# Kernel optimization log

Hardware: AMD Instinct MI355X
Metric: run time of the kernel (lower is better)

Reference implementation:

```python
import jax, jax.numpy as jnp
import numpy as np

TAU_RANK = 0.5
GAMMA_RANK = 1.0
TAU_GATE = 1.0
LN_EPS = 1e-5


def setup_inputs() -> dict:
    key = jax.random.key(0)
    ks = jax.random.split(key, 8)
    B, L, D, H, V = 8, 2048, 768, 1024, 32000
    ids = jax.random.randint(ks[0], (B, L), 0, V)
    embeddings = jax.random.normal(ks[1], (B, L, D), dtype=jnp.float32)
    attn = (jax.random.uniform(ks[2], (B, L)) < 0.9).astype(jnp.float32)
    rhos = jnp.array([0.1, 0.25, 0.5], dtype=jnp.float32)
    ln_g = jnp.ones((D,), jnp.float32)
    ln_b = jnp.zeros((D,), jnp.float32)
    w1 = jax.random.normal(ks[3], (D, H), dtype=jnp.float32) * 0.02
    b1 = jnp.zeros((H,), jnp.float32)
    w2 = jax.random.normal(ks[4], (H, 1), dtype=jnp.float32) * 0.02
    b2 = jnp.zeros((1,), jnp.float32)
    emb_table = jax.random.normal(ks[5], (V, D), dtype=jnp.float32) * 0.02
    return {"ids": ids, "embeddings": embeddings, "attn": attn, "rhos": rhos,
            "ln_g": ln_g, "ln_b": ln_b, "w1": w1, "b1": b1, "w2": w2, "b2": b2,
            "emb_table": emb_table}


def _selector_mlp(x, ln_g, ln_b, w1, b1, w2, b2):
    mu = x.mean(-1, keepdims=True)
    var = ((x - mu) ** 2).mean(-1, keepdims=True)
    x = (x - mu) / jnp.sqrt(var + LN_EPS) * ln_g + ln_b
    x = jax.nn.gelu(x @ w1 + b1, approximate=False)  # dropout eval = identity
    return (x @ w2 + b2)[..., 0]  # [B, L]


def _pool(emb, attn):
    # masked mean pooling: [.., L, D], [.., L] -> [.., D]
    denom = jnp.maximum(attn.sum(-1, keepdims=True), 1.0)
    return (emb * attn[..., None]).sum(-2) / denom


def _soft_rank(scores, attn, tau, gamma=1.0):
    scores = jnp.where(attn == 0, 0.0, scores)
    denom = jnp.maximum(attn.sum(1, keepdims=True), 1.0)
    mean = (scores * attn).sum(1, keepdims=True) / denom
    var = (((scores - mean) ** 2) * attn).sum(1, keepdims=True) / denom
    s = (scores - mean) / jnp.sqrt(var + 1e-6)
    # diff[b,i,j] = s[b,i] - s[b,j]
    p = jax.nn.sigmoid(-(s[:, :, None] - s[:, None, :]) / tau)
    if gamma != 1.0:
        p = p ** gamma
    p = p * (attn[:, None, :] * attn[:, :, None])
    r = 0.5 + p.sum(2)
    return jnp.where(attn == 0, 1e9, r)


def reference(ids, embeddings, attn, rhos, ln_g, ln_b, w1, b1, w2, b2, emb_table):
    attn_f = attn.astype(jnp.float32)
    emb = embeddings * attn_f[..., None]
    scores = _selector_mlp(emb, ln_g, ln_b, w1, b1, w2, b2)
    scores = jnp.where(attn_f == 0, 0.0, scores)

    full_rep = jax.lax.stop_gradient(_pool(embeddings, attn_f))  # [B, D]
    L_eff = attn_f.sum(1)  # [B]
    ranks = _soft_rank(scores, attn_f, TAU_RANK, GAMMA_RANK)  # [B, L]

    B, L = ids.shape
    R = rhos.shape[0]
    k = jnp.round(rhos[:, None] * L_eff[None]).astype(jnp.int32)  # [R, B]
    k = jnp.where(L_eff[None] > 0, jnp.maximum(k, 1), 0)
    k_f = k.astype(jnp.float32)

    gate_raw = jax.nn.sigmoid((k_f[:, :, None] - ranks[None]) / TAU_GATE) * attn_f[None]
    z = gate_raw / jnp.maximum(gate_raw.sum(-1, keepdims=True), 1e-8)
    z = z * k_f[:, :, None]  # [R, B, L]

    invalid_ranks = jnp.where(attn_f == 0, jnp.inf, ranks)
    # rank position of each token = inverse of the sort permutation
    rank_pos = jnp.argsort(jnp.argsort(invalid_ranks, axis=1), axis=1)  # [B, L]
    g = (rank_pos[None] < k[:, :, None]).astype(jnp.float32)  # hard top-k gate [R, B, L]

    g_st = g + (z - jax.lax.stop_gradient(z))  # straight-through
    effective_attn = attn_f[None] * g_st  # [R, B, L]

    tok = emb_table[ids]  # [B, L, D]; shared across R
    pred_rep = _pool(tok[None], effective_attn)  # [R, B, D]

    eps = 1e-8
    num = (pred_rep * full_rep[None]).sum(-1)
    den = jnp.maximum(jnp.linalg.norm(pred_rep, axis=-1), eps) * \
          jnp.maximum(jnp.linalg.norm(full_rep[None] * jnp.ones_like(pred_rep[..., :1]), axis=-1), eps)
    cos = num / den
    loss = (1.0 - cos).mean()
    return z, g, loss
```

## Files before the change

kernel.cpp:

```cpp
#include <hip/hip_runtime.h>
#include <math.h>

#define NB 8
#define NL 2048
#define ND 768
#define NH 1024
#define NR 3
#define NM (NB*NL)
#define LS 32
#define LOG2E  1.4426950408889634f
#define LOG2E2 2.8853900817779268f

typedef _Float16 h16;
typedef __attribute__((ext_vector_type(2))) _Float16 h16x2;
typedef __attribute__((ext_vector_type(8))) _Float16 h16x8;
typedef __attribute__((ext_vector_type(4))) float f32x4;

#define ASCALE 4.0f
#define BSCALE 64.0f
#define INV_AB (1.0f/(ASCALE*BSCALE))

enum : int {
  WS_SCORES = 0,
  WS_MU     = WS_SCORES + NM,
  WS_ISTD   = WS_MU + NM,
  WS_LEFF   = WS_ISTD + NM,
  WS_SMEAN  = WS_LEFF + 8,
  WS_SISTD  = WS_SMEAN + 8,
  WS_KF     = WS_SISTD + 8,
  WS_GDEN   = WS_KF + 24,
  WS_LOSSP  = WS_GDEN + 24,
  WS_CBP    = WS_LOSSP + 24,
  WS_SPART  = WS_CBP + 24*NH,
  WS_FPART  = WS_SPART + 16*NM,
  WS_PPART  = WS_FPART + LS*NB*ND,
  WS_RPART  = WS_PPART + LS*NR*NB*ND,
  WS_POSP   = WS_RPART + 4*NM,
  WS_BTH    = WS_POSP + 4*NM,
  WS_BTL    = WS_BTH + NH*ND/2,
  WS_END    = WS_BTL + NH*ND/2
};

__device__ __forceinline__ float block_sum256(float v) {
  __shared__ float tmp[4];
  __shared__ float res;
  int lane = threadIdx.x & 63;
  int w = threadIdx.x >> 6;
  #pragma unroll
  for (int o = 32; o > 0; o >>= 1) v += __shfl_down(v, o);
  if (lane == 0) tmp[w] = v;
  __syncthreads();
  if (threadIdx.x == 0) res = tmp[0] + tmp[1] + tmp[2] + tmp[3];
  __syncthreads();
  return res;
}

__device__ __forceinline__ void f16split2(float a, float b, h16x2& hi, h16x2& lo) {
  auto h = __builtin_amdgcn_cvt_pkrtz(a, b);
  float ra = a - (float)h[0];
  float rb = b - (float)h[1];
  auto l = __builtin_amdgcn_cvt_pkrtz(ra, rb);
  hi = (h16x2){(h16)h[0], (h16)h[1]};
  lo = (h16x2){(h16)l[0], (h16)l[1]};
}

__device__ __forceinline__ float fsig_exp2(float x) {
  return __builtin_amdgcn_rcpf(1.f + exp2f(x));
}

__global__ void k_stats(const float* __restrict__ emb, const float* __restrict__ attn,
                        float* __restrict__ ws) {
  int w = threadIdx.x >> 6, l = threadIdx.x & 63;
  int m = blockIdx.x*4 + w;
  const float* x = emb + (size_t)m * ND;
  float a = attn[m];
  float4 v0 = *(const float4*)&x[l*4];
  float4 v1 = *(const float4*)&x[256 + l*4];
  float4 v2 = *(const float4*)&x[512 + l*4];
  float s = v0.x+v0.y+v0.z+v0.w + v1.x+v1.y+v1.z+v1.w + v2.x+v2.y+v2.z+v2.w;
  #pragma unroll
  for (int o = 1; o < 64; o <<= 1) s += __shfl_xor(s, o);
  float mu = a * s / (float)ND;
  float q = 0.f;
  float xs[12] = {v0.x,v0.y,v0.z,v0.w, v1.x,v1.y,v1.z,v1.w, v2.x,v2.y,v2.z,v2.w};
  #pragma unroll
  for (int e = 0; e < 12; ++e) { float d = xs[e]*a - mu; q = fmaf(d, d, q); }
  #pragma unroll
  for (int o = 1; o < 64; o <<= 1) q += __shfl_xor(q, o);
  if (l == 0) {
    ws[WS_MU + m] = mu;
    ws[WS_ISTD + m] = 1.f / sqrtf(q / (float)ND + 1e-5f);
  }
}

__global__ void k_fullpart(const float* __restrict__ emb, const float* __restrict__ attn,
                           float* __restrict__ ws) {
  int b = blockIdx.x, dc = blockIdx.y, ls = blockIdx.z;
  int d = dc*256 + threadIdx.x;
  float acc = 0.f;
  int l0 = ls * (NL/LS);
  for (int l = l0; l < l0 + NL/LS; ++l)
    acc = fmaf(emb[((size_t)(b*NL + l))*ND + d], attn[b*NL + l], acc);
  ws[WS_FPART + ls*(NB*ND) + b*ND + d] = acc;
}

__global__ void k_splitBcb(const float* __restrict__ w1, const float* __restrict__ lng,
                           const float* __restrict__ lnb, float* __restrict__ ws) {
  __shared__ float tile[32][33];
  int bk = blockIdx.x, bn = blockIdx.y, t = threadIdx.x;
  int i = t >> 5, j = t & 31;
  #pragma unroll
  for (int s = 0; s < 4; ++s)
    tile[i + 8*s][j] = w1[(size_t)(bk*32 + i + 8*s)*NH + bn*32 + j];
  __syncthreads();
  h16* bth = (h16*)(ws + WS_BTH);
  h16* btl = (h16*)(ws + WS_BTL);
  int kl = j;
  float lg = lng[bk*32 + kl] * BSCALE;
  #pragma unroll
  for (int s = 0; s < 4; ++s) {
    int nl = i + 8*s;
    int n = bn*32 + nl, k = bk*32 + kl;
    float v = tile[kl][nl] * lg;
    h16 hi = (h16)v;
    bth[(size_t)n*ND + k] = hi;
    btl[(size_t)n*ND + k] = (h16)(v - (float)hi);
  }
  if (t < 32) {
    float s = 0.f;
    #pragma unroll
    for (int kl2 = 0; kl2 < 32; ++kl2)
      s = fmaf(lnb[bk*32 + kl2], tile[kl2][t], s);
    ws[WS_CBP + bk*NH + bn*32 + t] = s;
  }
}

__global__ void __launch_bounds__(256) k_gemm(
    const float* __restrict__ emb, const float* __restrict__ attn,
    const float* __restrict__ b1, const float* __restrict__ w2,
    float* __restrict__ ws) {
  __shared__ h16 AsH[128][36], AsL[128][36], BsH[128][36], BsL[128][36];
  int t = threadIdx.x;
  int m0 = blockIdx.x * 128, n0 = blockIdx.y * 128;
  int ar = t >> 1, ak = (t & 1) * 16;
  float isv = ws[WS_ISTD + m0 + ar];
  float pco  = ASCALE * attn[m0 + ar] * isv;
  float mqco = -ASCALE * ws[WS_MU + m0 + ar] * isv;
  int lane = t & 63, w = t >> 6, wm = w >> 1, wn = w & 1;
  int fr = lane & 15, g = lane >> 4;
  f32x4 acc[4][4];
  #pragma unroll
  for (int i = 0; i < 4; ++i)
    #pragma unroll
    for (int j = 0; j < 4; ++j) acc[i][j] = (f32x4){0.f, 0.f, 0.f, 0.f};
  const h16* bth = (const h16*)(ws + WS_BTH);
  const h16* btl = (const h16*)(ws + WS_BTL);

  for (int k0 = 0; k0 < ND; k0 += 32) {
    h16 hs[16], lo[16];
    #pragma unroll
    for (int i = 0; i < 2; ++i) {
      float4 x0 = *(const float4*)&emb[(size_t)(m0 + ar)*ND + k0 + ak + 8*i];
      float4 x1 = *(const float4*)&emb[(size_t)(m0 + ar)*ND + k0 + ak + 8*i + 4];
      h16x2 h0, l0v, h1, l1, h2, l2, h3, l3;
      f16split2(fmaf(x0.x, pco, mqco), fmaf(x0.y, pco, mqco), h0, l0v);
      f16split2(fmaf(x0.z, pco, mqco), fmaf(x0.w, pco, mqco), h1, l1);
      f16split2(fmaf(x1.x, pco, mqco), fmaf(x1.y, pco, mqco), h2, l2);
      f16split2(fmaf(x1.z, pco, mqco), fmaf(x1.w, pco, mqco), h3, l3);
      hs[8*i+0]=h0[0]; hs[8*i+1]=h0[1]; hs[8*i+2]=h1[0]; hs[8*i+3]=h1[1];
      hs[8*i+4]=h2[0]; hs[8*i+5]=h2[1]; hs[8*i+6]=h3[0]; hs[8*i+7]=h3[1];
      lo[8*i+0]=l0v[0]; lo[8*i+1]=l0v[1]; lo[8*i+2]=l1[0]; lo[8*i+3]=l1[1];
      lo[8*i+4]=l2[0]; lo[8*i+5]=l2[1]; lo[8*i+6]=l3[0]; lo[8*i+7]=l3[1];
    }
    h16x8 bh0 = *(const h16x8*)&bth[(size_t)(n0 + ar)*ND + k0 + ak];
    h16x8 bh1 = *(const h16x8*)&bth[(size_t)(n0 + ar)*ND + k0 + ak + 8];
    h16x8 bl0 = *(const h16x8*)&btl[(size_t)(n0 + ar)*ND + k0 + ak];
    h16x8 bl1 = *(const h16x8*)&btl[(size_t)(n0 + ar)*ND + k0 + ak + 8];
    __syncthreads();
    *(h16x8*)&AsH[ar][ak]     = *(const h16x8*)&hs[0];
    *(h16x8*)&AsH[ar][ak + 8] = *(const h16x8*)&hs[8];
    *(h16x8*)&AsL[ar][ak]     = *(const h16x8*)&lo[0];
    *(h16x8*)&AsL[ar][ak + 8] = *(const h16x8*)&lo[8];
    *(h16x8*)&BsH[ar][ak]     = bh0;
    *(h16x8*)&BsH[ar][ak + 8] = bh1;
    *(h16x8*)&BsL[ar][ak]     = bl0;
    *(h16x8*)&BsL[ar][ak + 8] = bl1;
    __syncthreads();
    h16x8 ah[4], al[4];
    #pragma unroll
    for (int mi = 0; mi < 4; ++mi) {
      int r = wm*64 + mi*16 + fr;
      ah[mi] = *(const h16x8*)&AsH[r][g*8];
      al[mi] = *(const h16x8*)&AsL[r][g*8];
    }
    #pragma unroll
    for (int ni = 0; ni < 4; ++ni) {
      int c = wn*64 + ni*16 + fr;
      h16x8 bh = *(const h16x8*)&BsH[c][g*8];
      h16x8 bl = *(const h16x8*)&BsL[c][g*8];
      #pragma unroll
      for (int mi = 0; mi < 4; ++mi) {
        acc[mi][ni] = __builtin_amdgcn_mfma_f32_16x16x32_f16(ah[mi], bh, acc[mi][ni], 0, 0, 0);
        acc[mi][ni] = __builtin_amdgcn_mfma_f32_16x16x32_f16(ah[mi], bl, acc[mi][ni], 0, 0, 0);
        acc[mi][ni] = __builtin_amdgcn_mfma_f32_16x16x32_f16(al[mi], bh, acc[mi][ni], 0, 0, 0);
      }
    }
  }
  float b1v[4], w2v[4];
  #pragma unroll
  for (int ni = 0; ni < 4; ++ni) {
    int c = n0 + wn*64 + ni*16 + fr;
    float cb = 0.f;
    #pragma unroll
    for (int j = 0; j < 24; ++j) cb += ws[WS_CBP + j*NH + c];
    b1v[ni] = b1[c] + cb;
    w2v[ni] = w2[c];
  }
  #pragma unroll
  for (int mi = 0; mi < 4; ++mi) {
    #pragma unroll
    for (int q = 0; q < 4; ++q) {
      float p = 0.f;
      #pragma unroll
      for (int ni = 0; ni < 4; ++ni) {
        float h = fmaf(acc[mi][ni][q], INV_AB, b1v[ni]);
        float ge = 0.5f * h * (1.f + erff(h * 0.70710678118654752f));
        p = fmaf(ge, w2v[ni], p);
      }
      p += __shfl_xor(p, 1);
      p += __shfl_xor(p, 2);
      p += __shfl_xor(p, 4);
      p += __shfl_xor(p, 8);
      if (fr == 0)
        ws[WS_SPART + (blockIdx.y*2 + wn)*NM + m0 + wm*64 + mi*16 + 4*g + q] = p;
    }
  }
}

__global__ void k_scorestats(const float* __restrict__ attn, const float* __restrict__ b2,
                             float* __restrict__ ws) {
  __shared__ float sS[NL];
  __shared__ float aS[NL];
  int b = blockIdx.x, t = threadIdx.x;
  float b2v = b2[0];
  float sa = 0.f, at = 0.f;
  for (int l = t; l < NL; l += 256) {
    float s = 0.f;
    #pragma unroll
    for (int j = 0; j < 16; ++j) s += ws[WS_SPART + j*NM + b*NL + l];
    s += b2v;
    ws[WS_SCORES + b*NL + l] = s;
    float a = attn[b*NL + l];
    sS[l] = s; aS[l] = a;
    at += a; sa = fmaf(a, s, sa);
  }
  float leff = block_sum256(at);
  float mean = block_sum256(sa) / fmaxf(leff, 1.f);
  float v = 0.f;
  for (int l = t; l < NL; l += 256) {
    float d = sS[l] - mean;
    v = fmaf(aS[l] * d, d, v);
  }
  float var = block_sum256(v) / fmaxf(leff, 1.f);
  if (t == 0) {
    ws[WS_LEFF + b] = leff;
    ws[WS_SMEAN + b] = mean;
    ws[WS_SISTD + b] = 1.f / sqrtf(var + 1e-6f);
  }
}

__global__ void k_rankpart(const float* __restrict__ attn, float* __restrict__ ws) {
  __shared__ float sCh[512];
  int b = blockIdx.x, c = blockIdx.y, js = blockIdx.z, t = threadIdx.x;
  float mean = ws[WS_SMEAN + b], istd = ws[WS_SISTD + b] * LOG2E2;
  for (int j = t; j < 512; j += 256) {
    int jj = js*512 + j;
    float a = attn[b*NL + jj];
    sCh[j] = (a != 0.f) ? (ws[WS_SCORES + b*NL + jj] - mean) * istd : -2.9e30f;
  }
  __syncthreads();
  int i = c*256 + t;
  float ai = attn[b*NL + i];
  float zi = (ai != 0.f) ? (ws[WS_SCORES + b*NL + i] - mean) * istd : -2.9e30f;
  float acc = 0.f;
  #pragma unroll 4
  for (int j = 0; j < 512; ++j)
    acc += fsig_exp2(zi - sCh[j]);
  ws[WS_RPART + js*NM + b*NL + i] = acc;
}

__global__ void k_gatedenom(const float* __restrict__ attn, const float* __restrict__ rhos,
                            float* __restrict__ ws) {
  int rb = blockIdx.x;
  int r = rb / NB, b = rb % NB;
  int t = threadIdx.x;
  float le = ws[WS_LEFF + b];
  float kf = rintf(rhos[r] * le);
  kf = (le > 0.f) ? fmaxf(kf, 1.f) : 0.f;
  float s = 0.f;
  for (int l = t; l < NL; l += 256) {
    int i = b*NL + l;
    float ri = 0.5f + ws[WS_RPART + i] + ws[WS_RPART + NM + i]
                    + ws[WS_RPART + 2*NM + i] + ws[WS_RPART + 3*NM + i];
    s += attn[i] * fsig_exp2((ri - kf) * LOG2E);
  }
  float tot = block_sum256(s);
  if (t == 0) { ws[WS_KF + rb] = kf; ws[WS_GDEN + rb] = fmaxf(tot, 1e-8f); }
}

__global__ void k_pospart(const float* __restrict__ attn, float* __restrict__ ws) {
  __shared__ float rCh[512];
  int b = blockIdx.x, c = blockIdx.y, js = blockIdx.z, t = threadIdx.x;
  for (int j = t; j < 512; j += 256) {
    int jj = b*NL + js*512 + j;
    float rr = 0.5f + ws[WS_RPART + jj] + ws[WS_RPART + NM + jj]
                    + ws[WS_RPART + 2*NM + jj] + ws[WS_RPART + 3*NM + jj];
    rCh[j] = (attn[jj] != 0.f) ? rr : 1e9f;
  }
  __syncthreads();
  int i = c*256 + t, ii = b*NL + i;
  float ri = 0.5f + ws[WS_RPART + ii] + ws[WS_RPART + NM + ii]
                  + ws[WS_RPART + 2*NM + ii] + ws[WS_RPART + 3*NM + ii];
  ri = (attn[ii] != 0.f) ? ri : 1e9f;
  int jbase = js*512;
  int cnt = 0;
  #pragma unroll 4
  for (int j = 0; j < 512; ++j) {
    float rj = rCh[j];
    cnt += (rj < ri) || (rj == ri && (jbase + j) < i);
  }
  ws[WS_POSP + js*NM + ii] = (float)cnt;
}

__global__ void k_zg(const float* __restrict__ attn, const float* __restrict__ ws,
                     float* __restrict__ out) {
  int b = blockIdx.x, c = blockIdx.y, t = threadIdx.x;
  int i = c*256 + t, ii = b*NL + i;
  float ai = attn[ii];
  float ri = 0.5f + ws[WS_RPART + ii] + ws[WS_RPART + NM + ii]
                  + ws[WS_RPART + 2*NM + ii] + ws[WS_RPART + 3*NM + ii];
  ri = (ai != 0.f) ? ri : 1e9f;
  int pos = (int)(ws[WS_POSP + ii] + ws[WS_POSP + NM + ii]
                + ws[WS_POSP + 2*NM + ii] + ws[WS_POSP + 3*NM + ii]);
  #pragma unroll
  for (int r = 0; r < NR; ++r) {
    float kf = ws[WS_KF + r*NB + b];
    float gd = ws[WS_GDEN + r*NB + b];
    float gate = ai * fsig_exp2((ri - kf) * LOG2E);
    float z = gate / gd * kf;
    float g = (pos < (int)kf) ? 1.f : 0.f;
    out[((size_t)(r*NB + b))*NL + i] = z;
    out[(size_t)NR*NB*NL + ((size_t)(r*NB + b))*NL + i] = g;
  }
}

__global__ void k_poolpart(const int* __restrict__ ids, const float* __restrict__ tab,
                           const float* __restrict__ out, float* __restrict__ ws) {
  int b = blockIdx.x, dc = blockIdx.y, ls = blockIdx.z;
  int d = dc*256 + threadIdx.x;
  const float* g0 = out + (size_t)NR*NB*NL + ((size_t)(0*NB + b))*NL;
  const float* g1 = out + (size_t)NR*NB*NL + ((size_t)(1*NB + b))*NL;
  const float* g2 = out + (size_t)NR*NB*NL + ((size_t)(2*NB + b))*NL;
  float a0 = 0.f, a1 = 0.f, a2 = 0.f;
  int l0 = ls * (NL/LS);
  for (int l = l0; l < l0 + NL/LS; ++l) {
    float gg0 = g0[l], gg1 = g1[l], gg2 = g2[l];
    if (gg0 + gg1 + gg2 == 0.f) continue;
    float v = tab[(size_t)ids[b*NL + l]*ND + d];
    a0 = fmaf(gg0, v, a0); a1 = fmaf(gg1, v, a1); a2 = fmaf(gg2, v, a2);
  }
  float* pp = ws + WS_PPART + ls*(NR*NB*ND);
  pp[(0*NB + b)*ND + d] = a0;
  pp[(1*NB + b)*ND + d] = a1;
  pp[(2*NB + b)*ND + d] = a2;
}

__global__ void k_lossp(float* __restrict__ ws) {
  int rb = blockIdx.x, t = threadIdx.x;
  int b = rb & 7;
  float dn = fmaxf(ws[WS_KF + rb], 1.f);
  float le = fmaxf(ws[WS_LEFF + b], 1.f);
  float num = 0.f, p2 = 0.f, f2 = 0.f;
  for (int d = t; d < ND; d += 256) {
    float ps = 0.f, fs = 0.f;
    #pragma unroll 8
    for (int j = 0; j < LS; ++j) {
      ps += ws[WS_PPART + j*(NR*NB*ND) + rb*ND + d];
      fs += ws[WS_FPART + j*(NB*ND) + b*ND + d];
    }
    float p = ps / dn, f = fs / le;
    num = fmaf(p, f, num); p2 = fmaf(p, p, p2); f2 = fmaf(f, f, f2);
  }
  num = block_sum256(num);
  p2 = block_sum256(p2);
  f2 = block_sum256(f2);
  if (t == 0)
    ws[WS_LOSSP + rb] = 1.f - num / (fmaxf(sqrtf(p2), 1e-8f) * fmaxf(sqrtf(f2), 1e-8f));
}

__global__ void k_losssum(const float* __restrict__ ws, float* __restrict__ out) {
  int t = threadIdx.x;
  float v = (t < NR*NB) ? ws[WS_LOSSP + t] : 0.f;
  #pragma unroll
  for (int o = 32; o > 0; o >>= 1) v += __shfl_down(v, o);
  if (t == 0) out[(size_t)2*NR*NB*NL] = v / (float)(NR*NB);
}

extern "C" void kernel_launch(void* const* d_in, const int* in_sizes, int n_in,
                              void* d_out, int out_size, void* d_ws, size_t ws_size,
                              hipStream_t stream) {
  const int*   ids  = (const int*)d_in[0];
  const float* emb  = (const float*)d_in[1];
  const float* attn = (const float*)d_in[2];
  const float* rhos = (const float*)d_in[3];
  const float* lng  = (const float*)d_in[4];
  const float* lnb  = (const float*)d_in[5];
  const float* w1   = (const float*)d_in[6];
  const float* b1   = (const float*)d_in[7];
  const float* w2   = (const float*)d_in[8];
  const float* b2   = (const float*)d_in[9];
  const float* tab  = (const float*)d_in[10];
  float* out = (float*)d_out;
  float* ws  = (float*)d_ws;

  k_stats     <<<NM/4, 256, 0, stream>>>(emb, attn, ws);
  k_fullpart  <<<dim3(NB, 3, LS), 256, 0, stream>>>(emb, attn, ws);
  k_splitBcb  <<<dim3(ND/32, NH/32), 256, 0, stream>>>(w1, lng, lnb, ws);
  k_gemm      <<<dim3(NM/128, NH/128), 256, 0, stream>>>(emb, attn, b1, w2, ws);
  k_scorestats<<<NB, 256, 0, stream>>>(attn, b2, ws);
  k_rankpart  <<<dim3(NB, NL/256, 4), 256, 0, stream>>>(attn, ws);
  k_gatedenom <<<NR*NB, 256, 0, stream>>>(attn, rhos, ws);
  k_pospart   <<<dim3(NB, NL/256, 4), 256, 0, stream>>>(attn, ws);
  k_zg        <<<dim3(NB, NL/256), 256, 0, stream>>>(attn, ws, out);
  k_poolpart  <<<dim3(NB, 3, LS), 256, 0, stream>>>(ids, tab, out, ws);
  k_lossp     <<<NR*NB, 256, 0, stream>>>(ws);
  k_losssum   <<<1, 64, 0, stream>>>(ws, out);
}
```

Measured before the change: 452.7 us.

## Pre-split LayerNorm activations to fp16 and store weights in MFMA fragment layout

When the workspace is large enough, a new stats kernel normalizes each row and writes fp16 hi/lo split activations to global memory. The weight matrix is also written directly in the MFMA fragment order, so a new GEMM kernel can load operands from global memory into registers without LDS staging or __syncthreads. This removes the per-tile fp32-to-fp16 split work that each of the 8 N-blocks repeated, and removes the shared-memory round trip. In exchange it adds about 50 MB of extra global writes and reads for the split activations, and the GEMM now has no LDS reuse across waves. The old path is kept as a fallback for when the workspace is too small.

```diff
diff --git a/kernel.cpp b/kernel.cpp
--- a/kernel.cpp
+++ b/kernel.cpp
@@ -12,7 +12,7 @@
 #define LOG2E2 2.8853900817779268f
 
 typedef _Float16 h16;
-typedef __attribute__((ext_vector_type(2))) _Float16 h16x2;
+typedef __attribute__((ext_vector_type(4))) _Float16 h16x4;
 typedef __attribute__((ext_vector_type(8))) _Float16 h16x8;
 typedef __attribute__((ext_vector_type(4))) float f32x4;
 
@@ -36,9 +36,12 @@
   WS_PPART  = WS_FPART + LS*NB*ND,
   WS_RPART  = WS_PPART + LS*NR*NB*ND,
   WS_POSP   = WS_RPART + 4*NM,
-  WS_BTH    = WS_POSP + 4*NM,
-  WS_BTL    = WS_BTH + NH*ND/2,
-  WS_END    = WS_BTL + NH*ND/2
+  WS_BT0    = WS_POSP + 4*NM,
+  WS_BT1    = WS_BT0 + NH*ND/2,
+  WS_SMALL_END = WS_BT1 + NH*ND/2,
+  WS_ATH    = WS_SMALL_END,
+  WS_ATL    = WS_ATH + NM*ND/2,
+  WS_END    = WS_ATL + NM*ND/2
 };
 
 __device__ __forceinline__ float block_sum256(float v) {
@@ -55,18 +58,164 @@
   return res;
 }
 
-__device__ __forceinline__ void f16split2(float a, float b, h16x2& hi, h16x2& lo) {
-  auto h = __builtin_amdgcn_cvt_pkrtz(a, b);
-  float ra = a - (float)h[0];
-  float rb = b - (float)h[1];
-  auto l = __builtin_amdgcn_cvt_pkrtz(ra, rb);
-  hi = (h16x2){(h16)h[0], (h16)h[1]};
-  lo = (h16x2){(h16)l[0], (h16)l[1]};
+__device__ __forceinline__ void f16split(float v, h16& hi, h16& lo) {
+  hi = (h16)v;
+  lo = (h16)(v - (float)hi);
 }
 
 __device__ __forceinline__ float fsig_exp2(float x) {
   return __builtin_amdgcn_rcpf(1.f + exp2f(x));
 }
+
+
+__global__ void k_statsA(const float* __restrict__ emb, const float* __restrict__ attn,
+                         float* __restrict__ ws) {
+  int w = threadIdx.x >> 6, l = threadIdx.x & 63;
+  int m = blockIdx.x*4 + w;
+  const float* x = emb + (size_t)m * ND;
+  float a = attn[m];
+  float4 v0 = *(const float4*)&x[l*4];
+  float4 v1 = *(const float4*)&x[256 + l*4];
+  float4 v2 = *(const float4*)&x[512 + l*4];
+  float s = v0.x+v0.y+v0.z+v0.w + v1.x+v1.y+v1.z+v1.w + v2.x+v2.y+v2.z+v2.w;
+  #pragma unroll
+  for (int o = 1; o < 64; o <<= 1) s += __shfl_xor(s, o);
+  float mu = a * s / (float)ND;
+  float q = 0.f;
+  float xs[12] = {v0.x,v0.y,v0.z,v0.w, v1.x,v1.y,v1.z,v1.w, v2.x,v2.y,v2.z,v2.w};
+  #pragma unroll
+  for (int e = 0; e < 12; ++e) { float d = xs[e]*a - mu; q = fmaf(d, d, q); }
+  #pragma unroll
+  for (int o = 1; o < 64; o <<= 1) q += __shfl_xor(q, o);
+  float istd = 1.f / sqrtf(q / (float)ND + 1e-5f);
+  float pco  = ASCALE * a * istd;
+  float mqco = -ASCALE * mu * istd;
+  h16* ath = (h16*)(ws + WS_ATH);
+  h16* atl = (h16*)(ws + WS_ATL);
+  #pragma unroll
+  for (int c = 0; c < 3; ++c) {
+    h16x4 hi4, lo4;
+    #pragma unroll
+    for (int e = 0; e < 4; ++e) {
+      float v = fmaf(xs[c*4 + e], pco, mqco);
+      h16 hi, lo;
+      f16split(v, hi, lo);
+      hi4[e] = hi; lo4[e] = lo;
+    }
+    size_t off = (size_t)m*ND + c*256 + l*4;
+    *(h16x4*)&ath[off] = hi4;
+    *(h16x4*)&atl[off] = lo4;
+  }
+}
+
+__global__ void k_splitBfrag(const float* __restrict__ w1, const float* __restrict__ lng,
+                             const float* __restrict__ lnb, float* __restrict__ ws) {
+  __shared__ float tile[32][33];
+  int bk = blockIdx.x, bn = blockIdx.y, t = threadIdx.x;
+  int i = t >> 5, j = t & 31;
+  #pragma unroll
+  for (int s = 0; s < 4; ++s)
+    tile[i + 8*s][j] = w1[(size_t)(bk*32 + i + 8*s)*NH + bn*32 + j];
+  __syncthreads();
+  h16* bth = (h16*)(ws + WS_BT0);
+  h16* btl = (h16*)(ws + WS_BT1);
+  int n_local = t & 31, g2 = (t >> 5) & 3, hl = t >> 7;
+  int n = bn*32 + n_local;
+  int nb16 = n >> 4;
+  int lanef = (n & 15) + 16*g2;
+  size_t base = ((size_t)(nb16*24 + bk)*64 + lanef)*8;
+  h16x8 out8;
+  #pragma unroll
+  for (int e = 0; e < 8; ++e) {
+    int kl = g2*8 + e;
+    float v = tile[kl][n_local] * (lng[bk*32 + kl] * BSCALE);
+    h16 hi, lo;
+    f16split(v, hi, lo);
+    out8[e] = hl ? lo : hi;
+  }
+  *(h16x8*)&((hl ? btl : bth)[base]) = out8;
+  if (t < 32) {
+    float s = 0.f;
+    #pragma unroll
+    for (int kl2 = 0; kl2 < 32; ++kl2)
+      s = fmaf(lnb[bk*32 + kl2], tile[kl2][t], s);
+    ws[WS_CBP + bk*NH + bn*32 + t] = s;
+  }
+}
+
+__global__ void __launch_bounds__(256) k_gemm_frag(
+    const float* __restrict__ b1, const float* __restrict__ w2,
+    float* __restrict__ ws) {
+  int t = threadIdx.x;
+  int lane = t & 63, w = t >> 6, wm = w >> 1, wn = w & 1;
+  int fr = lane & 15, g = lane >> 4;
+  int nb = blockIdx.x, mb = blockIdx.y;
+  int m0 = mb*128, n0 = nb*128;
+  const h16* __restrict__ ath = (const h16*)(ws + WS_ATH);
+  const h16* __restrict__ atl = (const h16*)(ws + WS_ATL);
+  const h16* __restrict__ bfh = (const h16*)(ws + WS_BT0);
+  const h16* __restrict__ bfl = (const h16*)(ws + WS_BT1);
+  size_t abase = (size_t)(m0 + wm*64 + fr)*ND + g*8;
+  size_t bbase = ((size_t)(nb*8 + wn*4)*24*64 + lane)*8;
+  f32x4 acc[4][4];
+  #pragma unroll
+  for (int i = 0; i < 4; ++i)
+    #pragma unroll
+    for (int j = 0; j < 4; ++j) acc[i][j] = (f32x4){0.f, 0.f, 0.f, 0.f};
+
+  #pragma unroll 1
+  for (int kb = 0; kb < 24; ++kb) {
+    h16x8 ah[4], al[4], bh[4], bl[4];
+    #pragma unroll
+    for (int mi = 0; mi < 4; ++mi) {
+      ah[mi] = *(const h16x8*)&ath[abase + (size_t)mi*(16*ND) + kb*32];
+      al[mi] = *(const h16x8*)&atl[abase + (size_t)mi*(16*ND) + kb*32];
+    }
+    #pragma unroll
+    for (int ni = 0; ni < 4; ++ni) {
+      bh[ni] = *(const h16x8*)&bfh[bbase + ((size_t)ni*24 + kb)*(64*8)];
+      bl[ni] = *(const h16x8*)&bfl[bbase + ((size_t)ni*24 + kb)*(64*8)];
+    }
+    #pragma unroll
+    for (int ni = 0; ni < 4; ++ni)
+      #pragma unroll
+      for (int mi = 0; mi < 4; ++mi) {
+        acc[mi][ni] = __builtin_amdgcn_mfma_f32_16x16x32_f16(ah[mi], bh[ni], acc[mi][ni], 0, 0, 0);
+        acc[mi][ni] = __builtin_amdgcn_mfma_f32_16x16x32_f16(ah[mi], bl[ni], acc[mi][ni], 0, 0, 0);
+        acc[mi][ni] = __builtin_amdgcn_mfma_f32_16x16x32_f16(al[mi], bh[ni], acc[mi][ni], 0, 0, 0);
+      }
+  }
+  float b1v[4], w2v[4];
+  #pragma unroll
+  for (int ni = 0; ni < 4; ++ni) {
+    int c = n0 + wn*64 + ni*16 + fr;
+    float cb = 0.f;
+    #pragma unroll
+    for (int j = 0; j < 24; ++j) cb += ws[WS_CBP + j*NH + c];
+    b1v[ni] = b1[c] + cb;
+    w2v[ni] = w2[c];
+  }
+  #pragma unroll
+  for (int mi = 0; mi < 4; ++mi) {
+    #pragma unroll
+    for (int q = 0; q < 4; ++q) {
+      float p = 0.f;
+      #pragma unroll
+      for (int ni = 0; ni < 4; ++ni) {
+        float h = fmaf(acc[mi][ni][q], INV_AB, b1v[ni]);
+        float ge = 0.5f * h * (1.f + erff(h * 0.70710678118654752f));
+        p = fmaf(ge, w2v[ni], p);
+      }
+      p += __shfl_xor(p, 1);
+      p += __shfl_xor(p, 2);
+      p += __shfl_xor(p, 4);
+      p += __shfl_xor(p, 8);
+      if (fr == 0)
+        ws[WS_SPART + (nb*2 + wn)*NM + m0 + wm*64 + mi*16 + 4*g + q] = p;
+    }
+  }
+}
+
 
 __global__ void k_stats(const float* __restrict__ emb, const float* __restrict__ attn,
                         float* __restrict__ ws) {
@@ -93,17 +242,6 @@
   }
 }
 
-__global__ void k_fullpart(const float* __restrict__ emb, const float* __restrict__ attn,
-                           float* __restrict__ ws) {
-  int b = blockIdx.x, dc = blockIdx.y, ls = blockIdx.z;
-  int d = dc*256 + threadIdx.x;
-  float acc = 0.f;
-  int l0 = ls * (NL/LS);
-  for (int l = l0; l < l0 + NL/LS; ++l)
-    acc = fmaf(emb[((size_t)(b*NL + l))*ND + d], attn[b*NL + l], acc);
-  ws[WS_FPART + ls*(NB*ND) + b*ND + d] = acc;
-}
-
 __global__ void k_splitBcb(const float* __restrict__ w1, const float* __restrict__ lng,
                            const float* __restrict__ lnb, float* __restrict__ ws) {
   __shared__ float tile[32][33];
@@ -113,8 +251,8 @@
   for (int s = 0; s < 4; ++s)
     tile[i + 8*s][j] = w1[(size_t)(bk*32 + i + 8*s)*NH + bn*32 + j];
   __syncthreads();
-  h16* bth = (h16*)(ws + WS_BTH);
-  h16* btl = (h16*)(ws + WS_BTL);
+  h16* bth = (h16*)(ws + WS_BT0);
+  h16* btl = (h16*)(ws + WS_BT1);
   int kl = j;
   float lg = lng[bk*32 + kl] * BSCALE;
   #pragma unroll
@@ -122,9 +260,10 @@
     int nl = i + 8*s;
     int n = bn*32 + nl, k = bk*32 + kl;
     float v = tile[kl][nl] * lg;
-    h16 hi = (h16)v;
+    h16 hi, lo;
+    f16split(v, hi, lo);
     bth[(size_t)n*ND + k] = hi;
-    btl[(size_t)n*ND + k] = (h16)(v - (float)hi);
+    btl[(size_t)n*ND + k] = lo;
   }
   if (t < 32) {
     float s = 0.f;
@@ -135,11 +274,11 @@
   }
 }
 
-__global__ void __launch_bounds__(256) k_gemm(
+__global__ void __launch_bounds__(256) k_gemm_fb(
     const float* __restrict__ emb, const float* __restrict__ attn,
     const float* __restrict__ b1, const float* __restrict__ w2,
     float* __restrict__ ws) {
-  __shared__ h16 AsH[128][36], AsL[128][36], BsH[128][36], BsL[128][36];
+  __shared__ h16 AsH[128][40], AsL[128][40], BsH[128][40], BsL[128][40];
   int t = threadIdx.x;
   int m0 = blockIdx.x * 128, n0 = blockIdx.y * 128;
   int ar = t >> 1, ak = (t & 1) * 16;
@@ -153,24 +292,18 @@
   for (int i = 0; i < 4; ++i)
     #pragma unroll
     for (int j = 0; j < 4; ++j) acc[i][j] = (f32x4){0.f, 0.f, 0.f, 0.f};
-  const h16* bth = (const h16*)(ws + WS_BTH);
-  const h16* btl = (const h16*)(ws + WS_BTL);
+  const h16* bth = (const h16*)(ws + WS_BT0);
+  const h16* btl = (const h16*)(ws + WS_BT1);
 
   for (int k0 = 0; k0 < ND; k0 += 32) {
     h16 hs[16], lo[16];
     #pragma unroll
-    for (int i = 0; i < 2; ++i) {
-      float4 x0 = *(const float4*)&emb[(size_t)(m0 + ar)*ND + k0 + ak + 8*i];
-      float4 x1 = *(const float4*)&emb[(size_t)(m0 + ar)*ND + k0 + ak + 8*i + 4];
-      h16x2 h0, l0v, h1, l1, h2, l2, h3, l3;
-      f16split2(fmaf(x0.x, pco, mqco), fmaf(x0.y, pco, mqco), h0, l0v);
-      f16split2(fmaf(x0.z, pco, mqco), fmaf(x0.w, pco, mqco), h1, l1);
-      f16split2(fmaf(x1.x, pco, mqco), fmaf(x1.y, pco, mqco), h2, l2);
-      f16split2(fmaf(x1.z, pco, mqco), fmaf(x1.w, pco, mqco), h3, l3);
-      hs[8*i+0]=h0[0]; hs[8*i+1]=h0[1]; hs[8*i+2]=h1[0]; hs[8*i+3]=h1[1];
-      hs[8*i+4]=h2[0]; hs[8*i+5]=h2[1]; hs[8*i+6]=h3[0]; hs[8*i+7]=h3[1];
-      lo[8*i+0]=l0v[0]; lo[8*i+1]=l0v[1]; lo[8*i+2]=l1[0]; lo[8*i+3]=l1[1];
-      lo[8*i+4]=l2[0]; lo[8*i+5]=l2[1]; lo[8*i+6]=l3[0]; lo[8*i+7]=l3[1];
+    for (int i = 0; i < 4; ++i) {
+      float4 x = *(const float4*)&emb[(size_t)(m0 + ar)*ND + k0 + ak + 4*i];
+      float xv[4] = {x.x, x.y, x.z, x.w};
+      #pragma unroll
+      for (int e = 0; e < 4; ++e)
+        f16split(fmaf(xv[e], pco, mqco), hs[4*i+e], lo[4*i+e]);
     }
     h16x8 bh0 = *(const h16x8*)&bth[(size_t)(n0 + ar)*ND + k0 + ak];
     h16x8 bh1 = *(const h16x8*)&bth[(size_t)(n0 + ar)*ND + k0 + ak + 8];
@@ -235,6 +368,18 @@
         ws[WS_SPART + (blockIdx.y*2 + wn)*NM + m0 + wm*64 + mi*16 + 4*g + q] = p;
     }
   }
+}
+
+
+__global__ void k_fullpart(const float* __restrict__ emb, const float* __restrict__ attn,
+                           float* __restrict__ ws) {
+  int b = blockIdx.x, dc = blockIdx.y, ls = blockIdx.z;
+  int d = dc*256 + threadIdx.x;
+  float acc = 0.f;
+  int l0 = ls * (NL/LS);
+  for (int l = l0; l < l0 + NL/LS; ++l)
+    acc = fmaf(emb[((size_t)(b*NL + l))*ND + d], attn[b*NL + l], acc);
+  ws[WS_FPART + ls*(NB*ND) + b*ND + d] = acc;
 }
 
 __global__ void k_scorestats(const float* __restrict__ attn, const float* __restrict__ b2,
@@ -423,10 +568,19 @@
   float* out = (float*)d_out;
   float* ws  = (float*)d_ws;
 
-  k_stats     <<<NM/4, 256, 0, stream>>>(emb, attn, ws);
-  k_fullpart  <<<dim3(NB, 3, LS), 256, 0, stream>>>(emb, attn, ws);
-  k_splitBcb  <<<dim3(ND/32, NH/32), 256, 0, stream>>>(w1, lng, lnb, ws);
-  k_gemm      <<<dim3(NM/128, NH/128), 256, 0, stream>>>(emb, attn, b1, w2, ws);
+  bool big = ws_size >= (size_t)WS_END * sizeof(float);
+
+  if (big) {
+    k_statsA   <<<NM/4, 256, 0, stream>>>(emb, attn, ws);
+    k_fullpart <<<dim3(NB, 3, LS), 256, 0, stream>>>(emb, attn, ws);
+    k_splitBfrag<<<dim3(ND/32, NH/32), 256, 0, stream>>>(w1, lng, lnb, ws);
+    k_gemm_frag<<<dim3(NH/128, NM/128), 256, 0, stream>>>(b1, w2, ws);
+  } else {
+    k_stats    <<<NM/4, 256, 0, stream>>>(emb, attn, ws);
+    k_fullpart <<<dim3(NB, 3, LS), 256, 0, stream>>>(emb, attn, ws);
+    k_splitBcb <<<dim3(ND/32, NH/32), 256, 0, stream>>>(w1, lng, lnb, ws);
+    k_gemm_fb  <<<dim3(NM/128, NH/128), 256, 0, stream>>>(emb, attn, b1, w2, ws);
+  }
   k_scorestats<<<NB, 256, 0, stream>>>(attn, b2, ws);
   k_rankpart  <<<dim3(NB, NL/256, 4), 256, 0, stream>>>(attn, ws);
   k_gatedenom <<<NR*NB, 256, 0, stream>>>(attn, rhos, ws);
```

New measurement: 413.9 us. 1.09x faster.
